# Performance work log

Hardware: AMD Instinct MI355X
Metric: run time of the kernel (lower is better)

The kernel has to match this reference:

```python
import jax, jax.numpy as jnp
import numpy as np

H = 4  # num_heads

def setup_inputs() -> dict:
    key = jax.random.key(0)
    ks = jax.random.split(key, 9)
    B, S, D = 8, 2048, 256
    x = jax.random.normal(ks[0], (B, S, D), dtype=jnp.float32)
    scale = 1.0 / np.sqrt(D)
    Wq = jax.random.normal(ks[1], (D, D), dtype=jnp.float32) * scale
    bq = jnp.zeros((D,), dtype=jnp.float32)
    Wk = jax.random.normal(ks[2], (D, D), dtype=jnp.float32) * scale
    bk = jnp.zeros((D,), dtype=jnp.float32)
    Wv = jax.random.normal(ks[3], (D, D), dtype=jnp.float32) * scale
    bv = jnp.zeros((D,), dtype=jnp.float32)
    Wo = jax.random.normal(ks[4], (D, D), dtype=jnp.float32) * scale
    bo = jnp.zeros((D,), dtype=jnp.float32)
    return {"x": x, "Wq": Wq, "bq": bq, "Wk": Wk, "bk": bk,
            "Wv": Wv, "bv": bv, "Wo": Wo, "bo": bo}

def reference(x, Wq, bq, Wk, bk, Wv, bv, Wo, bo):
    B, S, D = x.shape
    hd = D // H
    inv_scale = 1.0 / jnp.sqrt(jnp.asarray(hd, x.dtype))
    # projections: torch Linear is x @ W.T + b; weights here stored as (D, D) used as x @ W + b
    def split_heads(t):
        return t.reshape(B, S, H, hd).transpose(0, 2, 1, 3)  # [B,H,S,hd]
    Q = split_heads(x @ Wq + bq)
    K = split_heads(x @ Wk + bk)
    V = split_heads(x @ Wv + bv)
    scores = jnp.einsum('bhqd,bhkd->bhqk', Q, K) * inv_scale  # [B,H,S,S]
    attn = jax.nn.softmax(scores, axis=-1)
    # dropout is identity in eval mode
    ctx = jnp.einsum('bhqk,bhkd->bhqd', attn, V)
    ctx = ctx.transpose(0, 2, 1, 3).reshape(B, S, D)
    return ctx @ Wo + bo
```

## Files before the change

kernel.cpp:

```cpp
#include <hip/hip_runtime.h>


typedef unsigned short u16;
typedef __bf16 bf16x8 __attribute__((ext_vector_type(8)));
typedef float  f32x4  __attribute__((ext_vector_type(4)));
typedef unsigned int u32x4 __attribute__((ext_vector_type(4)));
typedef unsigned int u32x2 __attribute__((ext_vector_type(2)));

#define LOG2E   1.4426950408889634f
#define ATTN_SC (0.125f * LOG2E)
#define PSTR    2097152
#define WPSTR   32768
#define WZSTR   65536

__device__ __forceinline__ u16 f2b(float f) {
  unsigned u = __builtin_bit_cast(unsigned, f);
  u += 0x7FFFu + ((u >> 16) & 1u);
  return (u16)(u >> 16);
}
__device__ __forceinline__ float b2f(u16 b) {
  return __builtin_bit_cast(float, (unsigned)b << 16);
}
__device__ __forceinline__ unsigned pack_trunc(float a, float b) {
  return (__builtin_bit_cast(unsigned, a) >> 16) | (__builtin_bit_cast(unsigned, b) & 0xFFFF0000u);
}
__device__ __forceinline__ unsigned pack_rne(float a, float b) {
  return (unsigned)f2b(a) | ((unsigned)f2b(b) << 16);
}
__device__ __forceinline__ f32x4 mfma16(bf16x8 a, bf16x8 b, f32x4 c) {
  return __builtin_amdgcn_mfma_f32_16x16x32_bf16(a, b, c, 0, 0, 0);
}
__device__ __forceinline__ void cp16(const u16* g, u16* l) {
  __builtin_amdgcn_global_load_lds((const __attribute__((address_space(1))) void*)g,
                                   (__attribute__((address_space(3))) void*)l, 16, 0, 0);
}

template <typename T>
__global__ __launch_bounds__(256) void prep(const T* __restrict__ x,
                                            const T* __restrict__ W0, const T* __restrict__ W1,
                                            const T* __restrict__ W2, const T* __restrict__ W3,
                                            const T* __restrict__ b0, const T* __restrict__ b1,
                                            const T* __restrict__ b2, const T* __restrict__ b3,
                                            u16* __restrict__ xp, u16* __restrict__ WTp,
                                            float* __restrict__ biasf) {
  int bid = blockIdx.x;
  if (bid < 4096) {
    int i0 = (bid * 256 + threadIdx.x) * 4;
    int row = i0 >> 8, col = i0 & 255;
    int p = col >> 7, pc = col & 127;
    u16* o = xp + (size_t)p * PSTR + (size_t)row * 128 + pc;
#pragma unroll
    for (int j = 0; j < 4; ++j) {
      if constexpr (sizeof(T) == 4) o[j] = f2b((float)x[i0 + j]);
      else                          o[j] = (u16)x[i0 + j];
    }
  } else {
    bid -= 4096;
    const int z = bid >> 8;
    const T* W = z == 0 ? W0 : z == 1 ? W1 : z == 2 ? W2 : W3;
    const T* b = z == 0 ? b0 : z == 1 ? b1 : z == 2 ? b2 : b3;
    int idx = (bid & 255) * 256 + threadIdx.x;
    int k = idx >> 8, n = idx & 255;
    u16 wb;
    if constexpr (sizeof(T) == 4) wb = f2b((float)W[k * 256 + n]);
    else                          wb = (u16)W[k * 256 + n];
    WTp[z * WZSTR + (k >> 7) * WPSTR + n * 128 + (k & 127)] = wb;
    if (idx < 256) {
      float bv;
      if constexpr (sizeof(T) == 4) bv = (float)b[idx];
      else                          bv = b2f((u16)b[idx]);
      biasf[z * 256 + idx] = bv;
    }
  }
}

__device__ __forceinline__ void gemm_body(const u16* Ab, const u16* Bb,
                                          u16* Al, u16* Bl, f32x4 acc[2][4], int tid) {
  const int w = tid >> 6, lane = tid & 63;
  const int l16 = lane & 15, quad = lane >> 4;
#pragma unroll
  for (int p = 0; p < 2; ++p) {
    __syncthreads();
    const u16* Ap = Ab + (size_t)p * PSTR;
    const u16* Bp = Bb + p * WPSTR;
#pragma unroll
    for (int i = 0; i < 8; ++i) {
      int slot = i * 256 + w * 64 + lane;
      int row = slot >> 4, pc = slot & 15, c = pc ^ (row & 15);
      cp16(Ap + (size_t)row * 128 + c * 8, Al + (i * 256 + w * 64) * 8);
    }
#pragma unroll
    for (int i = 0; i < 4; ++i) {
      int slot = i * 256 + w * 64 + lane;
      int row = slot >> 4, pc = slot & 15, c = pc ^ (row & 15);
      cp16(Bp + (size_t)row * 128 + c * 8, Bl + (i * 256 + w * 64) * 8);
    }
    __syncthreads();
#pragma unroll
    for (int kc = 0; kc < 4; ++kc) {
      bf16x8 a0 = *(const bf16x8*)&Al[(w * 32 + l16) * 128 + (((kc * 4 + quad) ^ l16)) * 8];
      bf16x8 a1 = *(const bf16x8*)&Al[(w * 32 + 16 + l16) * 128 + (((kc * 4 + quad) ^ l16)) * 8];
#pragma unroll
      for (int nb = 0; nb < 4; ++nb) {
        bf16x8 b = *(const bf16x8*)&Bl[(nb * 16 + l16) * 128 + (((kc * 4 + quad) ^ l16)) * 8];
        acc[0][nb] = mfma16(a0, b, acc[0][nb]);
        acc[1][nb] = mfma16(a1, b, acc[1][nb]);
      }
    }
  }
}

__global__ __launch_bounds__(256) void qkv_gemm(const u16* __restrict__ xp, const u16* __restrict__ WTp,
                                                const float* __restrict__ biasf,
                                                u16* __restrict__ Qw, u16* __restrict__ Kw,
                                                u16* __restrict__ VTg) {
  __shared__ __align__(16) u16 Al[128 * 128];
  __shared__ __align__(16) u16 Bl[64 * 128];
  const int tid = threadIdx.x, w = tid >> 6, lane = tid & 63;
  const int l16 = lane & 15, quad = lane >> 4;
  const int z = blockIdx.z, n0 = blockIdx.y * 64, m0 = blockIdx.x * 128;
  f32x4 acc[2][4];
#pragma unroll
  for (int mm = 0; mm < 2; ++mm)
#pragma unroll
    for (int nb = 0; nb < 4; ++nb) acc[mm][nb] = (f32x4){0.f, 0.f, 0.f, 0.f};

  gemm_body(xp + (size_t)m0 * 128, WTp + z * WZSTR + n0 * 128, Al, Bl, acc, tid);

  const float* bp = biasf + z * 256;
  const int bb = m0 >> 11, s0 = m0 & 2047, h = blockIdx.y;
  if (z < 2) {
    u16* dst = (z == 0) ? Qw : Kw;
    const float sc = (z == 0) ? ATTN_SC : 1.0f;
#pragma unroll
    for (int mm = 0; mm < 2; ++mm)
#pragma unroll
      for (int nb = 0; nb < 4; ++nb) {
        int d = nb * 16 + l16;
        float bv = bp[n0 + d];
#pragma unroll
        for (int r = 0; r < 4; ++r) {
          int s = s0 + w * 32 + mm * 16 + quad * 4 + r;
          dst[(((size_t)(bb * 4 + h) * 2048) + s) * 64 + d] = f2b((acc[mm][nb][r] + bv) * sc);
        }
      }
  } else {
    __syncthreads();
#pragma unroll
    for (int mm = 0; mm < 2; ++mm)
#pragma unroll
      for (int nb = 0; nb < 4; ++nb) {
        int d = nb * 16 + l16;
        float bv = bp[n0 + d];
        f32x4 v = acc[mm][nb];
        u32x2 dd = { pack_rne(v[0] + bv, v[1] + bv), pack_rne(v[2] + bv, v[3] + bv) };
        int cch = w * 4 + mm * 2 + (quad >> 1);
        *(u32x2*)&Bl[d * 128 + ((cch ^ (d & 15))) * 8 + (quad & 1) * 4] = dd;
      }
    __syncthreads();
#pragma unroll
    for (int i = 0; i < 4; ++i) {
      int slot = i * 256 + tid;
      int d = slot >> 4, pc = slot & 15;
      u32x4 vv = *(const u32x4*)&Bl[d * 128 + ((pc ^ (d & 15))) * 8];
      *(u32x4*)(VTg + (((size_t)(bb * 4 + h) * 64) + d) * 2048 + s0 + pc * 8) = vv;
    }
  }
}

template <bool OUT_BF16>
__global__ __launch_bounds__(256) void out_gemm(const u16* __restrict__ ctxp, const u16* __restrict__ WTp,
                                                const float* __restrict__ bo, void* __restrict__ outv) {
  __shared__ __align__(16) u16 Al[128 * 128];
  __shared__ __align__(16) u16 Bl[64 * 128];
  const int tid = threadIdx.x, w = tid >> 6, lane = tid & 63;
  const int l16 = lane & 15, quad = lane >> 4;
  const int n0 = blockIdx.y * 64, m0 = blockIdx.x * 128;
  f32x4 acc[2][4];
#pragma unroll
  for (int mm = 0; mm < 2; ++mm)
#pragma unroll
    for (int nb = 0; nb < 4; ++nb) acc[mm][nb] = (f32x4){0.f, 0.f, 0.f, 0.f};

  gemm_body(ctxp + (size_t)m0 * 128, WTp + 3 * WZSTR + n0 * 128, Al, Bl, acc, tid);

#pragma unroll
  for (int mm = 0; mm < 2; ++mm)
#pragma unroll
    for (int nb = 0; nb < 4; ++nb) {
      int n = n0 + nb * 16 + l16;
      float bv = bo[n];
#pragma unroll
      for (int r = 0; r < 4; ++r) {
        size_t m = m0 + w * 32 + mm * 16 + quad * 4 + r;
        float v = acc[mm][nb][r] + bv;
        if constexpr (OUT_BF16) ((u16*)outv)[m * 256 + n] = f2b(v);
        else                    ((float*)outv)[m * 256 + n] = v;
      }
    }
}

__global__ __launch_bounds__(256, 4) void attn(const u16* __restrict__ Q, const u16* __restrict__ K,
                                               const u16* __restrict__ VT, u16* __restrict__ ctxp) {
  __shared__ __align__(16) u16 Kt[2][64 * 64];
  __shared__ __align__(16) u16 VTt[2][64 * 64];
  __shared__ __align__(16) u16 Pt[4][16 * 64];
  const int tid = threadIdx.x;
  const int w = tid >> 6, lane = tid & 63;
  const int l16 = lane & 15, quad = lane >> 4;
  const int bh = blockIdx.y, q0 = blockIdx.x * 64;
  const u16* Qp = Q + (size_t)bh * 2048 * 64;
  const u16* Kp = K + (size_t)bh * 2048 * 64;
  const u16* Vp = VT + (size_t)bh * 64 * 2048;
  u16* Ptw = Pt[w];

  bf16x8 qf0, qf1;
  {
    int qrow = q0 + w * 16 + l16;
    qf0 = *(const bf16x8*)(Qp + (size_t)qrow * 64 + quad * 8);
    qf1 = *(const bf16x8*)(Qp + (size_t)qrow * 64 + 32 + quad * 8);
  }

  f32x4 acc[4];
#pragma unroll
  for (int nb = 0; nb < 4; ++nb) acc[nb] = (f32x4){0.f, 0.f, 0.f, 0.f};
  float dn = 0.f;

  const int sl0 = w * 64 + lane, sl1 = 256 + w * 64 + lane;
  const int r0 = sl0 >> 3, c0 = (sl0 & 7) ^ (r0 & 7);
  const int r1 = sl1 >> 3, c1 = (sl1 & 7) ^ (r1 & 7);

#define STAGE(kt_, buf_)                                                              \
  do {                                                                                \
    cp16(Kp + (size_t)((kt_) * 64 + r0) * 64 + c0 * 8, &Kt[buf_][(w * 64) * 8]);      \
    cp16(Kp + (size_t)((kt_) * 64 + r1) * 64 + c1 * 8, &Kt[buf_][(256 + w * 64) * 8]);\
    cp16(Vp + (size_t)r0 * 2048 + (kt_) * 64 + c0 * 8, &VTt[buf_][(w * 64) * 8]);     \
    cp16(Vp + (size_t)r1 * 2048 + (kt_) * 64 + c1 * 8, &VTt[buf_][(256 + w * 64) * 8]);\
  } while (0)

  STAGE(0, 0);

  for (int kt = 0; kt < 32; ++kt) {
    const int buf = kt & 1;
    __builtin_amdgcn_s_waitcnt(0x0F70 );
    __asm__ __volatile__("" ::: "memory");
    __builtin_amdgcn_s_barrier();
    __asm__ __volatile__("" ::: "memory");
    if (kt < 31) STAGE(kt + 1, buf ^ 1);

    const u16* KtB = Kt[buf];
    const u16* VtB = VTt[buf];

    bf16x8 vbr[2][4];
#pragma unroll
    for (int m = 0; m < 2; ++m)
#pragma unroll
      for (int nbD = 0; nbD < 4; ++nbD)
        vbr[m][nbD] = *(const bf16x8*)&VtB[(nbD * 16 + l16) * 64 + (((m * 4 + quad) ^ (l16 & 7))) * 8];

    f32x4 st[4];
#pragma unroll
    for (int nb = 0; nb < 4; ++nb) st[nb] = (f32x4){0.f, 0.f, 0.f, 0.f};
#pragma unroll
    for (int kc = 0; kc < 2; ++kc) {
      bf16x8 qb = kc ? qf1 : qf0;
#pragma unroll
      for (int nbK = 0; nbK < 4; ++nbK) {
        bf16x8 a = *(const bf16x8*)&KtB[(nbK * 16 + l16) * 64 + (((kc * 4 + quad) ^ (l16 & 7))) * 8];
        st[nbK] = mfma16(a, qb, st[nbK]);
      }
    }

#pragma unroll
    for (int nbK = 0; nbK < 4; ++nbK) {
      float p0 = exp2f(st[nbK][0]), p1 = exp2f(st[nbK][1]);
      float p2 = exp2f(st[nbK][2]), p3 = exp2f(st[nbK][3]);
      dn += (p0 + p1) + (p2 + p3);
      u32x2 dd = { pack_trunc(p0, p1), pack_trunc(p2, p3) };
      int cch = nbK * 2 + (quad >> 1);
      *(u32x2*)&Ptw[l16 * 64 + ((cch ^ (l16 & 7))) * 8 + (quad & 1) * 4] = dd;
    }

#pragma unroll
    for (int m = 0; m < 2; ++m) {
      bf16x8 pb = *(const bf16x8*)&Ptw[l16 * 64 + (((m * 4 + quad) ^ (l16 & 7))) * 8];
#pragma unroll
      for (int nbD = 0; nbD < 4; ++nbD)
        acc[nbD] = mfma16(vbr[m][nbD], pb, acc[nbD]);
    }
  }
#undef STAGE

  dn += __shfl_xor(dn, 16);
  dn += __shfl_xor(dn, 32);
  float linv = 1.0f / dn;

  __asm__ __volatile__("" ::: "memory");
  __builtin_amdgcn_s_barrier();
  __asm__ __volatile__("" ::: "memory");
#pragma unroll
  for (int nbD = 0; nbD < 4; ++nbD) {
    f32x4 v = acc[nbD];
    u32x2 dd = { pack_rne(v[0] * linv, v[1] * linv), pack_rne(v[2] * linv, v[3] * linv) };
    int cch = nbD * 2 + (quad >> 1);
    *(u32x2*)&Ptw[l16 * 64 + ((cch ^ (l16 & 7))) * 8 + (quad & 1) * 4] = dd;
  }
  const int bb = bh >> 2, h = bh & 3;
  const int p = h >> 1, pcol = (h & 1) * 64;
#pragma unroll
  for (int cc = 0; cc < 2; ++cc) {
    int slot = cc * 64 + lane;
    int row = slot >> 3, pc = slot & 7;
    u32x4 vv = *(const u32x4*)&Ptw[row * 64 + ((pc ^ (row & 7))) * 8];
    size_t m = (size_t)bb * 2048 + q0 + w * 16 + row;
    *(u32x4*)&ctxp[(size_t)p * PSTR + m * 128 + pcol + pc * 8] = vv;
  }
}

extern "C" void kernel_launch(void* const* d_in, const int* in_sizes, int n_in,
                              void* d_out, int out_size, void* d_ws, size_t ws_size,
                              hipStream_t stream) {
  bool f32in = true;
  {
    void* basep = nullptr; size_t sz = 0;
    hipError_t e = hipMemGetAddressRange((hipDeviceptr_t*)&basep, &sz, (hipDeviceptr_t)d_in[0]);
    if (e == hipSuccess && sz > 0) f32in = sz >= (size_t)in_sizes[0] * 4;
    else f32in = false;
  }

  char* ws = (char*)d_ws;
  u16*   xp    = (u16*)(ws + 0);
  u16*   ctxp  = xp;
  u16*   WTp   = (u16*)(ws + 8388608);
  float* biasf = (float*)(ws + 8912896);
  u16*   Qw    = (u16*)(ws + 8916992);
  u16*   Kw    = (u16*)(ws + 17305600);
  u16*   VTg   = (u16*)(ws + 25694208);

  dim3 blk(256);
  if (f32in) {
    prep<float><<<5120, blk, 0, stream>>>(
        (const float*)d_in[0],
        (const float*)d_in[1], (const float*)d_in[3], (const float*)d_in[5], (const float*)d_in[7],
        (const float*)d_in[2], (const float*)d_in[4], (const float*)d_in[6], (const float*)d_in[8],
        xp, WTp, biasf);
  } else {
    prep<u16><<<5120, blk, 0, stream>>>(
        (const u16*)d_in[0],
        (const u16*)d_in[1], (const u16*)d_in[3], (const u16*)d_in[5], (const u16*)d_in[7],
        (const u16*)d_in[2], (const u16*)d_in[4], (const u16*)d_in[6], (const u16*)d_in[8],
        xp, WTp, biasf);
  }
  qkv_gemm<<<dim3(128, 4, 3), blk, 0, stream>>>(xp, WTp, biasf, Qw, Kw, VTg);
  attn<<<dim3(32, 32), blk, 0, stream>>>(Qw, Kw, VTg, ctxp);
  if (f32in) out_gemm<false><<<dim3(128, 4), blk, 0, stream>>>(ctxp, WTp, biasf + 3 * 256, d_out);
  else       out_gemm<true ><<<dim3(128, 4), blk, 0, stream>>>(ctxp, WTp, biasf + 3 * 256, d_out);
}
```

Measured before the change: 166.9 us.

## Enlarge per-wave tiles in QKV GEMM and attention for register reuse

The QKV GEMM block tile grows from 128 to 256 rows, so each wave computes a 64x64 output with 4x4 MFMA fragments, and the grid halves. The attention kernel drops to 128 threads per block, with each wave handling 32 query rows in two groups. Each K/V fragment read from LDS then feeds twice as many MFMAs. The shared GEMM body is inlined separately into each kernel. The cost is higher register and LDS use per block and fewer blocks or waves in flight, which reduces occupancy and latency hiding. Attention also drops its pre-store barrier, which appears safe because each wave now writes only its own Pt slice.

```diff
diff --git a/kernel.cpp b/kernel.cpp
--- a/kernel.cpp
+++ b/kernel.cpp
@@ -74,17 +74,30 @@
   }
 }
 
-__device__ __forceinline__ void gemm_body(const u16* Ab, const u16* Bb,
-                                          u16* Al, u16* Bl, f32x4 acc[2][4], int tid) {
-  const int w = tid >> 6, lane = tid & 63;
+__global__ __launch_bounds__(256, 2) void qkv_gemm(const u16* __restrict__ xp, const u16* __restrict__ WTp,
+                                                   const float* __restrict__ biasf,
+                                                   u16* __restrict__ Qw, u16* __restrict__ Kw,
+                                                   u16* __restrict__ VTg) {
+  __shared__ __align__(16) u16 Al[256 * 128];
+  __shared__ __align__(16) u16 Bl[64 * 128];
+  const int tid = threadIdx.x, w = tid >> 6, lane = tid & 63;
   const int l16 = lane & 15, quad = lane >> 4;
+  const int z = blockIdx.z, n0 = blockIdx.y * 64, m0 = blockIdx.x * 256;
+  const u16* Ab = xp + (size_t)m0 * 128;
+  const u16* Bb = WTp + z * WZSTR + (size_t)n0 * 128;
+  f32x4 acc[4][4];
+#pragma unroll
+  for (int mm = 0; mm < 4; ++mm)
+#pragma unroll
+    for (int nb = 0; nb < 4; ++nb) acc[mm][nb] = (f32x4){0.f, 0.f, 0.f, 0.f};
+
 #pragma unroll
   for (int p = 0; p < 2; ++p) {
     __syncthreads();
     const u16* Ap = Ab + (size_t)p * PSTR;
     const u16* Bp = Bb + p * WPSTR;
 #pragma unroll
-    for (int i = 0; i < 8; ++i) {
+    for (int i = 0; i < 16; ++i) {
       int slot = i * 256 + w * 64 + lane;
       int row = slot >> 4, pc = slot & 15, c = pc ^ (row & 15);
       cp16(Ap + (size_t)row * 128 + c * 8, Al + (i * 256 + w * 64) * 8);
@@ -98,34 +111,21 @@
     __syncthreads();
 #pragma unroll
     for (int kc = 0; kc < 4; ++kc) {
-      bf16x8 a0 = *(const bf16x8*)&Al[(w * 32 + l16) * 128 + (((kc * 4 + quad) ^ l16)) * 8];
-      bf16x8 a1 = *(const bf16x8*)&Al[(w * 32 + 16 + l16) * 128 + (((kc * 4 + quad) ^ l16)) * 8];
-#pragma unroll
-      for (int nb = 0; nb < 4; ++nb) {
-        bf16x8 b = *(const bf16x8*)&Bl[(nb * 16 + l16) * 128 + (((kc * 4 + quad) ^ l16)) * 8];
-        acc[0][nb] = mfma16(a0, b, acc[0][nb]);
-        acc[1][nb] = mfma16(a1, b, acc[1][nb]);
-      }
-    }
-  }
-}
-
-__global__ __launch_bounds__(256) void qkv_gemm(const u16* __restrict__ xp, const u16* __restrict__ WTp,
-                                                const float* __restrict__ biasf,
-                                                u16* __restrict__ Qw, u16* __restrict__ Kw,
-                                                u16* __restrict__ VTg) {
-  __shared__ __align__(16) u16 Al[128 * 128];
-  __shared__ __align__(16) u16 Bl[64 * 128];
-  const int tid = threadIdx.x, w = tid >> 6, lane = tid & 63;
-  const int l16 = lane & 15, quad = lane >> 4;
-  const int z = blockIdx.z, n0 = blockIdx.y * 64, m0 = blockIdx.x * 128;
-  f32x4 acc[2][4];
-#pragma unroll
-  for (int mm = 0; mm < 2; ++mm)
-#pragma unroll
-    for (int nb = 0; nb < 4; ++nb) acc[mm][nb] = (f32x4){0.f, 0.f, 0.f, 0.f};
-
-  gemm_body(xp + (size_t)m0 * 128, WTp + z * WZSTR + n0 * 128, Al, Bl, acc, tid);
+      int ch = ((kc * 4 + quad) ^ l16) * 8;
+      bf16x8 a[4], b[4];
+#pragma unroll
+      for (int mm = 0; mm < 4; ++mm)
+        a[mm] = *(const bf16x8*)&Al[(w * 64 + mm * 16 + l16) * 128 + ch];
+#pragma unroll
+      for (int nb = 0; nb < 4; ++nb)
+        b[nb] = *(const bf16x8*)&Bl[(nb * 16 + l16) * 128 + ch];
+#pragma unroll
+      for (int mm = 0; mm < 4; ++mm)
+#pragma unroll
+        for (int nb = 0; nb < 4; ++nb)
+          acc[mm][nb] = mfma16(a[mm], b[nb], acc[mm][nb]);
+    }
+  }
 
   const float* bp = biasf + z * 256;
   const int bb = m0 >> 11, s0 = m0 & 2047, h = blockIdx.y;
@@ -133,36 +133,36 @@
     u16* dst = (z == 0) ? Qw : Kw;
     const float sc = (z == 0) ? ATTN_SC : 1.0f;
 #pragma unroll
-    for (int mm = 0; mm < 2; ++mm)
+    for (int mm = 0; mm < 4; ++mm)
 #pragma unroll
       for (int nb = 0; nb < 4; ++nb) {
         int d = nb * 16 + l16;
         float bv = bp[n0 + d];
 #pragma unroll
         for (int r = 0; r < 4; ++r) {
-          int s = s0 + w * 32 + mm * 16 + quad * 4 + r;
+          int s = s0 + w * 64 + mm * 16 + quad * 4 + r;
           dst[(((size_t)(bb * 4 + h) * 2048) + s) * 64 + d] = f2b((acc[mm][nb][r] + bv) * sc);
         }
       }
   } else {
     __syncthreads();
 #pragma unroll
-    for (int mm = 0; mm < 2; ++mm)
+    for (int mm = 0; mm < 4; ++mm)
 #pragma unroll
       for (int nb = 0; nb < 4; ++nb) {
         int d = nb * 16 + l16;
         float bv = bp[n0 + d];
         f32x4 v = acc[mm][nb];
         u32x2 dd = { pack_rne(v[0] + bv, v[1] + bv), pack_rne(v[2] + bv, v[3] + bv) };
-        int cch = w * 4 + mm * 2 + (quad >> 1);
-        *(u32x2*)&Bl[d * 128 + ((cch ^ (d & 15))) * 8 + (quad & 1) * 4] = dd;
-      }
-    __syncthreads();
-#pragma unroll
-    for (int i = 0; i < 4; ++i) {
+        int cch = w * 8 + mm * 2 + (quad >> 1);
+        *(u32x2*)&Al[d * 256 + ((cch ^ (d & 31))) * 8 + (quad & 1) * 4] = dd;
+      }
+    __syncthreads();
+#pragma unroll
+    for (int i = 0; i < 8; ++i) {
       int slot = i * 256 + tid;
-      int d = slot >> 4, pc = slot & 15;
-      u32x4 vv = *(const u32x4*)&Bl[d * 128 + ((pc ^ (d & 15))) * 8];
+      int d = slot >> 5, pc = slot & 31;
+      u32x4 vv = *(const u32x4*)&Al[d * 256 + ((pc ^ (d & 31))) * 8];
       *(u32x4*)(VTg + (((size_t)(bb * 4 + h) * 64) + d) * 2048 + s0 + pc * 8) = vv;
     }
   }
@@ -176,14 +176,45 @@
   const int tid = threadIdx.x, w = tid >> 6, lane = tid & 63;
   const int l16 = lane & 15, quad = lane >> 4;
   const int n0 = blockIdx.y * 64, m0 = blockIdx.x * 128;
+  const u16* Ab = ctxp + (size_t)m0 * 128;
+  const u16* Bb = WTp + 3 * WZSTR + (size_t)n0 * 128;
   f32x4 acc[2][4];
 #pragma unroll
   for (int mm = 0; mm < 2; ++mm)
 #pragma unroll
     for (int nb = 0; nb < 4; ++nb) acc[mm][nb] = (f32x4){0.f, 0.f, 0.f, 0.f};
 
-  gemm_body(ctxp + (size_t)m0 * 128, WTp + 3 * WZSTR + n0 * 128, Al, Bl, acc, tid);
-
+#pragma unroll
+  for (int p = 0; p < 2; ++p) {
+    __syncthreads();
+    const u16* Ap = Ab + (size_t)p * PSTR;
+    const u16* Bp = Bb + p * WPSTR;
+#pragma unroll
+    for (int i = 0; i < 8; ++i) {
+      int slot = i * 256 + w * 64 + lane;
+      int row = slot >> 4, pc = slot & 15, c = pc ^ (row & 15);
+      cp16(Ap + (size_t)row * 128 + c * 8, Al + (i * 256 + w * 64) * 8);
+    }
+#pragma unroll
+    for (int i = 0; i < 4; ++i) {
+      int slot = i * 256 + w * 64 + lane;
+      int row = slot >> 4, pc = slot & 15, c = pc ^ (row & 15);
+      cp16(Bp + (size_t)row * 128 + c * 8, Bl + (i * 256 + w * 64) * 8);
+    }
+    __syncthreads();
+#pragma unroll
+    for (int kc = 0; kc < 4; ++kc) {
+      int ch = ((kc * 4 + quad) ^ l16) * 8;
+      bf16x8 a0 = *(const bf16x8*)&Al[(w * 32 + l16) * 128 + ch];
+      bf16x8 a1 = *(const bf16x8*)&Al[(w * 32 + 16 + l16) * 128 + ch];
+#pragma unroll
+      for (int nb = 0; nb < 4; ++nb) {
+        bf16x8 b = *(const bf16x8*)&Bl[(nb * 16 + l16) * 128 + ch];
+        acc[0][nb] = mfma16(a0, b, acc[0][nb]);
+        acc[1][nb] = mfma16(a1, b, acc[1][nb]);
+      }
+    }
+  }
 #pragma unroll
   for (int mm = 0; mm < 2; ++mm)
 #pragma unroll
@@ -200,11 +231,11 @@
     }
 }
 
-__global__ __launch_bounds__(256, 4) void attn(const u16* __restrict__ Q, const u16* __restrict__ K,
+__global__ __launch_bounds__(128, 2) void attn(const u16* __restrict__ Q, const u16* __restrict__ K,
                                                const u16* __restrict__ VT, u16* __restrict__ ctxp) {
   __shared__ __align__(16) u16 Kt[2][64 * 64];
   __shared__ __align__(16) u16 VTt[2][64 * 64];
-  __shared__ __align__(16) u16 Pt[4][16 * 64];
+  __shared__ __align__(16) u16 Pt[2][2][16 * 64];
   const int tid = threadIdx.x;
   const int w = tid >> 6, lane = tid & 63;
   const int l16 = lane & 15, quad = lane >> 4;
@@ -212,30 +243,39 @@
   const u16* Qp = Q + (size_t)bh * 2048 * 64;
   const u16* Kp = K + (size_t)bh * 2048 * 64;
   const u16* Vp = VT + (size_t)bh * 64 * 2048;
-  u16* Ptw = Pt[w];
-
-  bf16x8 qf0, qf1;
-  {
-    int qrow = q0 + w * 16 + l16;
-    qf0 = *(const bf16x8*)(Qp + (size_t)qrow * 64 + quad * 8);
-    qf1 = *(const bf16x8*)(Qp + (size_t)qrow * 64 + 32 + quad * 8);
-  }
-
-  f32x4 acc[4];
-#pragma unroll
-  for (int nb = 0; nb < 4; ++nb) acc[nb] = (f32x4){0.f, 0.f, 0.f, 0.f};
-  float dn = 0.f;
-
-  const int sl0 = w * 64 + lane, sl1 = 256 + w * 64 + lane;
-  const int r0 = sl0 >> 3, c0 = (sl0 & 7) ^ (r0 & 7);
-  const int r1 = sl1 >> 3, c1 = (sl1 & 7) ^ (r1 & 7);
-
-#define STAGE(kt_, buf_)                                                              \
-  do {                                                                                \
-    cp16(Kp + (size_t)((kt_) * 64 + r0) * 64 + c0 * 8, &Kt[buf_][(w * 64) * 8]);      \
-    cp16(Kp + (size_t)((kt_) * 64 + r1) * 64 + c1 * 8, &Kt[buf_][(256 + w * 64) * 8]);\
-    cp16(Vp + (size_t)r0 * 2048 + (kt_) * 64 + c0 * 8, &VTt[buf_][(w * 64) * 8]);     \
-    cp16(Vp + (size_t)r1 * 2048 + (kt_) * 64 + c1 * 8, &VTt[buf_][(256 + w * 64) * 8]);\
+
+  bf16x8 qf[2][2];
+#pragma unroll
+  for (int g = 0; g < 2; ++g) {
+    int qrow = q0 + w * 32 + g * 16 + l16;
+    qf[g][0] = *(const bf16x8*)(Qp + (size_t)qrow * 64 + quad * 8);
+    qf[g][1] = *(const bf16x8*)(Qp + (size_t)qrow * 64 + 32 + quad * 8);
+  }
+
+  f32x4 acc[2][4];
+#pragma unroll
+  for (int g = 0; g < 2; ++g)
+#pragma unroll
+    for (int nb = 0; nb < 4; ++nb) acc[g][nb] = (f32x4){0.f, 0.f, 0.f, 0.f};
+  float dn[2] = {0.f, 0.f};
+
+  int srow[4], scol[4];
+#pragma unroll
+  for (int i = 0; i < 4; ++i) {
+    int slot = i * 128 + tid;
+    srow[i] = slot >> 3;
+    scol[i] = (slot & 7) ^ (srow[i] & 7);
+  }
+
+#define STAGE(kt_, buf_)                                                                   \
+  do {                                                                                     \
+    _Pragma("unroll")                                                                      \
+    for (int i = 0; i < 4; ++i) {                                                          \
+      cp16(Kp + (size_t)((kt_) * 64 + srow[i]) * 64 + scol[i] * 8,                         \
+           &Kt[buf_][(i * 128 + w * 64) * 8]);                                             \
+      cp16(Vp + (size_t)srow[i] * 2048 + (kt_) * 64 + scol[i] * 8,                         \
+           &VTt[buf_][(i * 128 + w * 64) * 8]);                                            \
+    }                                                                                      \
   } while (0)
 
   STAGE(0, 0);
@@ -258,61 +298,77 @@
       for (int nbD = 0; nbD < 4; ++nbD)
         vbr[m][nbD] = *(const bf16x8*)&VtB[(nbD * 16 + l16) * 64 + (((m * 4 + quad) ^ (l16 & 7))) * 8];
 
-    f32x4 st[4];
-#pragma unroll
-    for (int nb = 0; nb < 4; ++nb) st[nb] = (f32x4){0.f, 0.f, 0.f, 0.f};
+    f32x4 st[2][4];
+#pragma unroll
+    for (int g = 0; g < 2; ++g)
+#pragma unroll
+      for (int nb = 0; nb < 4; ++nb) st[g][nb] = (f32x4){0.f, 0.f, 0.f, 0.f};
 #pragma unroll
     for (int kc = 0; kc < 2; ++kc) {
-      bf16x8 qb = kc ? qf1 : qf0;
 #pragma unroll
       for (int nbK = 0; nbK < 4; ++nbK) {
         bf16x8 a = *(const bf16x8*)&KtB[(nbK * 16 + l16) * 64 + (((kc * 4 + quad) ^ (l16 & 7))) * 8];
-        st[nbK] = mfma16(a, qb, st[nbK]);
-      }
-    }
-
-#pragma unroll
-    for (int nbK = 0; nbK < 4; ++nbK) {
-      float p0 = exp2f(st[nbK][0]), p1 = exp2f(st[nbK][1]);
-      float p2 = exp2f(st[nbK][2]), p3 = exp2f(st[nbK][3]);
-      dn += (p0 + p1) + (p2 + p3);
-      u32x2 dd = { pack_trunc(p0, p1), pack_trunc(p2, p3) };
-      int cch = nbK * 2 + (quad >> 1);
-      *(u32x2*)&Ptw[l16 * 64 + ((cch ^ (l16 & 7))) * 8 + (quad & 1) * 4] = dd;
+        st[0][nbK] = mfma16(a, qf[0][kc], st[0][nbK]);
+        st[1][nbK] = mfma16(a, qf[1][kc], st[1][nbK]);
+      }
+    }
+
+#pragma unroll
+    for (int g = 0; g < 2; ++g) {
+      u16* Ptg = Pt[w][g];
+#pragma unroll
+      for (int nbK = 0; nbK < 4; ++nbK) {
+        float p0 = exp2f(st[g][nbK][0]), p1 = exp2f(st[g][nbK][1]);
+        float p2 = exp2f(st[g][nbK][2]), p3 = exp2f(st[g][nbK][3]);
+        dn[g] += (p0 + p1) + (p2 + p3);
+        u32x2 dd = { pack_trunc(p0, p1), pack_trunc(p2, p3) };
+        int cch = nbK * 2 + (quad >> 1);
+        *(u32x2*)&Ptg[l16 * 64 + ((cch ^ (l16 & 7))) * 8 + (quad & 1) * 4] = dd;
+      }
     }
 
 #pragma unroll
     for (int m = 0; m < 2; ++m) {
-      bf16x8 pb = *(const bf16x8*)&Ptw[l16 * 64 + (((m * 4 + quad) ^ (l16 & 7))) * 8];
-#pragma unroll
-      for (int nbD = 0; nbD < 4; ++nbD)
-        acc[nbD] = mfma16(vbr[m][nbD], pb, acc[nbD]);
+#pragma unroll
+      for (int g = 0; g < 2; ++g) {
+        bf16x8 pb = *(const bf16x8*)&Pt[w][g][l16 * 64 + (((m * 4 + quad) ^ (l16 & 7))) * 8];
+#pragma unroll
+        for (int nbD = 0; nbD < 4; ++nbD)
+          acc[g][nbD] = mfma16(vbr[m][nbD], pb, acc[g][nbD]);
+      }
     }
   }
 #undef STAGE
 
-  dn += __shfl_xor(dn, 16);
-  dn += __shfl_xor(dn, 32);
-  float linv = 1.0f / dn;
-
-  __asm__ __volatile__("" ::: "memory");
-  __builtin_amdgcn_s_barrier();
-  __asm__ __volatile__("" ::: "memory");
-#pragma unroll
-  for (int nbD = 0; nbD < 4; ++nbD) {
-    f32x4 v = acc[nbD];
-    u32x2 dd = { pack_rne(v[0] * linv, v[1] * linv), pack_rne(v[2] * linv, v[3] * linv) };
-    int cch = nbD * 2 + (quad >> 1);
-    *(u32x2*)&Ptw[l16 * 64 + ((cch ^ (l16 & 7))) * 8 + (quad & 1) * 4] = dd;
+  float linv[2];
+#pragma unroll
+  for (int g = 0; g < 2; ++g) {
+    float d = dn[g];
+    d += __shfl_xor(d, 16);
+    d += __shfl_xor(d, 32);
+    linv[g] = 1.0f / d;
+  }
+
+#pragma unroll
+  for (int g = 0; g < 2; ++g) {
+    u16* Ptg = Pt[w][g];
+#pragma unroll
+    for (int nbD = 0; nbD < 4; ++nbD) {
+      f32x4 v = acc[g][nbD];
+      u32x2 dd = { pack_rne(v[0] * linv[g], v[1] * linv[g]),
+                   pack_rne(v[2] * linv[g], v[3] * linv[g]) };
+      int cch = nbD * 2 + (quad >> 1);
+      *(u32x2*)&Ptg[l16 * 64 + ((cch ^ (l16 & 7))) * 8 + (quad & 1) * 4] = dd;
+    }
   }
   const int bb = bh >> 2, h = bh & 3;
   const int p = h >> 1, pcol = (h & 1) * 64;
 #pragma unroll
-  for (int cc = 0; cc < 2; ++cc) {
+  for (int cc = 0; cc < 4; ++cc) {
     int slot = cc * 64 + lane;
     int row = slot >> 3, pc = slot & 7;
-    u32x4 vv = *(const u32x4*)&Ptw[row * 64 + ((pc ^ (row & 7))) * 8];
-    size_t m = (size_t)bb * 2048 + q0 + w * 16 + row;
+    u32x4 vv = *(const u32x4*)&Pt[w][0][row * 64 + ((pc ^ (row & 7))) * 8];
+    size_t m = (size_t)bb * 2048 + q0 + w * 32 + row;
     *(u32x4*)&ctxp[(size_t)p * PSTR + m * 128 + pcol + pc * 8] = vv;
   }
 }
@@ -337,22 +393,21 @@
   u16*   Kw    = (u16*)(ws + 17305600);
   u16*   VTg   = (u16*)(ws + 25694208);
 
-  dim3 blk(256);
   if (f32in) {
-    prep<float><<<5120, blk, 0, stream>>>(
+    prep<float><<<5120, 256, 0, stream>>>(
         (const float*)d_in[0],
         (const float*)d_in[1], (const float*)d_in[3], (const float*)d_in[5], (const float*)d_in[7],
         (const float*)d_in[2], (const float*)d_in[4], (const float*)d_in[6], (const float*)d_in[8],
         xp, WTp, biasf);
   } else {
-    prep<u16><<<5120, blk, 0, stream>>>(
+    prep<u16><<<5120, 256, 0, stream>>>(
         (const u16*)d_in[0],
         (const u16*)d_in[1], (const u16*)d_in[3], (const u16*)d_in[5], (const u16*)d_in[7],
         (const u16*)d_in[2], (const u16*)d_in[4], (const u16*)d_in[6], (const u16*)d_in[8],
         xp, WTp, biasf);
   }
-  qkv_gemm<<<dim3(128, 4, 3), blk, 0, stream>>>(xp, WTp, biasf, Qw, Kw, VTg);
-  attn<<<dim3(32, 32), blk, 0, stream>>>(Qw, Kw, VTg, ctxp);
-  if (f32in) out_gemm<false><<<dim3(128, 4), blk, 0, stream>>>(ctxp, WTp, biasf + 3 * 256, d_out);
-  else       out_gemm<true ><<<dim3(128, 4), blk, 0, stream>>>(ctxp, WTp, biasf + 3 * 256, d_out);
-}
+  qkv_gemm<<<dim3(64, 4, 3), 256, 0, stream>>>(xp, WTp, biasf, Qw, Kw, VTg);
+  attn<<<dim3(32, 32), 128, 0, stream>>>(Qw, Kw, VTg, ctxp);
+  if (f32in) out_gemm<false><<<dim3(128, 4), 256, 0, stream>>>(ctxp, WTp, biasf + 3 * 256, d_out);
+  else       out_gemm<true ><<<dim3(128, 4), 256, 0, stream>>>(ctxp, WTp, biasf + 3 * 256, d_out);
+}
```

Measured after the change: 174.1 us. 1.04x slower.
